# Optimization experiments

Hardware: AMD Instinct MI355X
Metric: run time of the kernel (lower is better)

## Reference

```python
import jax, jax.numpy as jnp
import numpy as np

N_NODES = 100000
N_EDGES = 1600000
D = 128
N_GRAPHS = 8


def setup_inputs() -> dict:
    key = jax.random.key(0)
    ks = jax.random.split(key, 10)
    x = jax.random.normal(ks[0], (N_NODES, D), dtype=jnp.float32)
    src = jax.random.randint(ks[1], (N_EDGES,), 0, N_NODES)
    dst = jax.random.randint(ks[2], (N_EDGES,), 0, N_NODES)
    graph_ids = jnp.sort(jax.random.randint(ks[3], (N_NODES,), 0, N_GRAPHS))
    s = 1.0 / np.sqrt(D)
    W1 = jax.random.normal(ks[4], (D, D), dtype=jnp.float32) * s
    b1 = jnp.zeros((D,), dtype=jnp.float32)
    W2 = jax.random.normal(ks[5], (D, D), dtype=jnp.float32) * s
    b2 = jnp.zeros((D,), dtype=jnp.float32)
    prelu_a = jnp.full((1,), 0.25, dtype=jnp.float32)
    lin_W = jax.random.normal(ks[6], (D, 1), dtype=jnp.float32) * s
    lin_b = jnp.zeros((1,), dtype=jnp.float32)
    return {"x": x, "src": src, "dst": dst, "graph_ids": graph_ids,
            "W1": W1, "b1": b1, "W2": W2, "b2": b2,
            "prelu_a": prelu_a, "lin_W": lin_W, "lin_b": lin_b}


def _gcn_layer(h, src, dst, n_src, n_dst, W, b):
    # GraphConv with symmetric ('both') normalization: D^{-1/2} A D^{-1/2} H W + b
    h = h @ W                                      # [N, D] small GEMM
    m = h[src] * n_src[:, None]                    # [E, D] gather (irregular)
    agg = jax.ops.segment_sum(m, dst, num_segments=N_NODES)  # scatter-add
    return agg * n_dst[:, None] + b


def reference(x, src, dst, graph_ids, W1, b1, W2, b2, prelu_a, lin_W, lin_b):
    ones_e = jnp.ones((src.shape[0],), dtype=x.dtype)
    deg_out = jnp.maximum(jax.ops.segment_sum(ones_e, src, num_segments=N_NODES), 1.0)
    deg_in = jnp.maximum(jax.ops.segment_sum(ones_e, dst, num_segments=N_NODES), 1.0)
    n_src = jax.lax.rsqrt(deg_out)[src]            # per-edge source norm
    n_dst = jax.lax.rsqrt(deg_in)                  # per-node dest norm

    h = _gcn_layer(x, src, dst, n_src, n_dst, W1, b1)
    h = jax.nn.relu(h)
    h = _gcn_layer(h, src, dst, n_src, n_dst, W2, b2)
    h = jax.nn.relu(h)

    # dgl.mean_nodes: per-graph mean over nodes
    sums = jax.ops.segment_sum(h, graph_ids, num_segments=N_GRAPHS)   # [G, D]
    cnt = jax.ops.segment_sum(jnp.ones((N_NODES,), h.dtype), graph_ids,
                              num_segments=N_GRAPHS)
    pooled = sums / jnp.maximum(cnt, 1.0)[:, None]

    # PReLU (single shared slope) -> Linear -> Sigmoid
    pooled = jnp.where(pooled > 0, pooled, prelu_a[0] * pooled)
    out = jax.nn.sigmoid(pooled @ lin_W + lin_b)   # [G, 1]
    return out
```

## Files before the change

kernel.cpp:

```cpp
#include <hip/hip_runtime.h>
#include <hip/hip_bf16.h>

#define NN 100000
#define NE 1600000
#define DD 128
#define NG 8

#define BSH 8
#define KB 391
#define BMASK 255
#define PB 512
#define CHUNK 3125
#define SCAN_N (KB * PB)
#define GHB 98

typedef unsigned short u16;
typedef unsigned char u8;
typedef __attribute__((ext_vector_type(8))) short short8;
typedef __attribute__((ext_vector_type(4))) float f32x4;
typedef __attribute__((ext_vector_type(2))) float f32x2;

static __device__ __forceinline__ u16 f2bf(float f) {
  unsigned u = __float_as_uint(f);
  u += 0x7fffu + ((u >> 16) & 1);
  return (u16)(u >> 16);
}
static __device__ __forceinline__ u8 f2fp8(float f) {
  return (u8)(__builtin_amdgcn_cvt_pk_fp8_f32(f, f, 0, false) & 0xFF);
}

__global__ __launch_bounds__(256) void p1x(const int* __restrict__ src,
                                           const int* __restrict__ dst,
                                           int* __restrict__ countsS,
                                           int* __restrict__ countsD,
                                           const float* __restrict__ W1,
                                           const float* __restrict__ W2,
                                           u16* __restrict__ Wt1,
                                           u16* __restrict__ Wt2,
                                           const int* __restrict__ gid,
                                           int* __restrict__ cnt_part,
                                           float* __restrict__ pooled) {
  __shared__ int hs[KB], hd[KB];
  __shared__ int h8[NG];
  int t = threadIdx.x, b = blockIdx.x;
  if (b < PB) {
    for (int i = t; i < KB; i += 256) { hs[i] = 0; hd[i] = 0; }
    __syncthreads();
    int e0 = b * CHUNK;
    for (int i = t; i < CHUNK; i += 256) {
      atomicAdd(&hs[src[e0 + i] >> BSH], 1);
      atomicAdd(&hd[dst[e0 + i] >> BSH], 1);
    }
    __syncthreads();
    for (int i = t; i < KB; i += 256) {
      countsS[i * PB + b] = hs[i];
      countsD[i * PB + b] = hd[i];
    }
  } else if (b < PB + 128) {
    int i = (b - PB) * 256 + t;
    if (i < DD * DD) {
      int n = i >> 7, k = i & 127;
      Wt1[i] = f2bf(W1[k * DD + n]);
    } else {
      int i2 = i - DD * DD;
      int n = i2 >> 7, k = i2 & 127;
      Wt2[i2] = f2bf(W2[k * DD + n]);
    }
  } else if (b < PB + 128 + GHB) {
    int blk = b - PB - 128;
    if (t < NG) h8[t] = 0;
    __syncthreads();
    for (int i = blk * 256 + t; i < NN; i += GHB * 256)
      atomicAdd(&h8[gid[i]], 1);
    __syncthreads();
    if (t < NG) cnt_part[blk * NG + t] = h8[t];
  } else {
    for (int i = t; i < NG * DD; i += 256) pooled[i] = 0.f;
  }
}

__global__ __launch_bounds__(256) void scanA(int* __restrict__ countsS,
                                             int* __restrict__ countsD,
                                             int* __restrict__ totS,
                                             int* __restrict__ totD) {
  __shared__ int data[PB];
  __shared__ int part[256];
  int b = blockIdx.x;
  int isS = (b < KB);
  int k = isS ? b : b - KB;
  int* counts = isS ? countsS : countsD;
  int* tot = isS ? totS : totD;
  int t = threadIdx.x;
  int* c = counts + (size_t)k * PB;
  data[t] = c[t];
  data[t + 256] = c[t + 256];
  __syncthreads();
  int a0 = data[2 * t], a1 = data[2 * t + 1];
  int s = a0 + a1;
  part[t] = s;
  __syncthreads();
  for (int off = 1; off < 256; off <<= 1) {
    int v = (t >= off) ? part[t - off] : 0;
    __syncthreads();
    part[t] += v;
    __syncthreads();
  }
  int ex = part[t] - s;
  data[2 * t] = ex;
  data[2 * t + 1] = ex + a0;
  __syncthreads();
  c[t] = data[t];
  c[t + 256] = data[t + 256];
  if (t == 255) tot[k] = part[255];
}

__global__ __launch_bounds__(256) void p2x(const int* __restrict__ src,
                                           const int* __restrict__ dst,
                                           const int* __restrict__ countsS,
                                           const int* __restrict__ countsD,
                                           const int* __restrict__ totS,
                                           const int* __restrict__ totD,
                                           int* __restrict__ baseS,
                                           int* __restrict__ baseD,
                                           u8* __restrict__ recsS,
                                           unsigned* __restrict__ recsD) {
  __shared__ int data[512];
  __shared__ int part[256];
  __shared__ int bS[KB + 1], bD[KB + 1];
  __shared__ int curS[KB], curD[KB];
  int t = threadIdx.x, blk = blockIdx.x;
#pragma unroll
  for (int pass = 0; pass < 2; ++pass) {
    const int* tot = pass ? totD : totS;
    int* bb = pass ? bD : bS;
    data[t] = (t < KB) ? tot[t] : 0;
    data[t + 256] = (t + 256 < KB) ? tot[t + 256] : 0;
    __syncthreads();
    int a0 = data[2 * t], a1 = data[2 * t + 1];
    int s = a0 + a1;
    part[t] = s;
    __syncthreads();
    for (int off = 1; off < 256; off <<= 1) {
      int v = (t >= off) ? part[t - off] : 0;
      __syncthreads();
      part[t] += v;
      __syncthreads();
    }
    int ex = part[t] - s;
    int i0 = 2 * t, i1 = 2 * t + 1;
    if (i0 <= KB) bb[i0] = ex;
    if (i1 <= KB) bb[i1] = ex + a0;
    __syncthreads();
  }
  for (int i = t; i < KB; i += 256) {
    curS[i] = countsS[i * PB + blk] + bS[i];
    curD[i] = countsD[i * PB + blk] + bD[i];
  }
  if (blk == 0) {
    for (int i = t; i <= KB; i += 256) {
      baseS[i] = bS[i];
      baseD[i] = bD[i];
    }
  }
  __syncthreads();
  int e0 = blk * CHUNK;
  for (int i = t; i < CHUNK; i += 256) {
    int s = src[e0 + i];
    int d = dst[e0 + i];
    int ps = atomicAdd(&curS[s >> BSH], 1);
    recsS[ps] = (u8)(s & BMASK);
    int pd = atomicAdd(&curD[d >> BSH], 1);
    recsD[pd] = (unsigned)s | ((unsigned)(d & BMASK) << 17);
  }
}

__global__ __launch_bounds__(256) void sd_p3x(const u8* __restrict__ recsS,
                                              const int* __restrict__ baseS,
                                              float* __restrict__ rs_out,
                                              const float* __restrict__ x,
                                              u8* __restrict__ bufA,
                                              const unsigned* __restrict__ recsD,
                                              const int* __restrict__ baseD,
                                              int* __restrict__ csr_src,
                                              int* __restrict__ cursor_end,
                                              int* __restrict__ deg_in,
                                              float* __restrict__ rs_in) {
  __shared__ int hist[256];
  __shared__ int part[256];
  __shared__ float rsl[256];
  int t = threadIdx.x;
  if (blockIdx.x < KB) {
    int k = blockIdx.x;
    int rbeg = baseS[k];
    int rend = baseS[k + 1];
    hist[t] = 0;
    __syncthreads();
    for (int i = rbeg + t; i < rend; i += 256) atomicAdd(&hist[recsS[i]], 1);
    __syncthreads();
    int nbase = k << BSH;
    int n = nbase + t;
    float rv = rsqrtf(fmaxf((float)hist[t], 1.f));
    rsl[t] = rv;
    if (n < NN) rs_out[n] = rv;
    __syncthreads();
    for (int i = t; i < 256 * 16; i += 256) {
      int row = i >> 4, c = i & 15;
      int node = nbase + row;
      if (node >= NN) break;
      float w = rsl[row];
      const float4* p = (const float4*)(x + (size_t)node * DD + c * 8);
      float4 a = p[0], b = p[1];
      int lo = 0, hi = 0;
      lo = __builtin_amdgcn_cvt_pk_fp8_f32(a.x * w, a.y * w, lo, false);
      lo = __builtin_amdgcn_cvt_pk_fp8_f32(a.z * w, a.w * w, lo, true);
      hi = __builtin_amdgcn_cvt_pk_fp8_f32(b.x * w, b.y * w, hi, false);
      hi = __builtin_amdgcn_cvt_pk_fp8_f32(b.z * w, b.w * w, hi, true);
      *(uint2*)(bufA + (size_t)node * DD + c * 8) = make_uint2((unsigned)lo, (unsigned)hi);
    }
  } else {
    int k = blockIdx.x - KB;
    int rbeg = baseD[k];
    int rend = baseD[k + 1];
    hist[t] = 0;
    __syncthreads();
    for (int i = rbeg + t; i < rend; i += 256) atomicAdd(&hist[recsD[i] >> 17], 1);
    __syncthreads();
    int h = hist[t];
    part[t] = h;
    __syncthreads();
    for (int off = 1; off < 256; off <<= 1) {
      int v = (t >= off) ? part[t - off] : 0;
      __syncthreads();
      part[t] += v;
      __syncthreads();
    }
    int run = rbeg + part[t] - h;
    int n = (k << BSH) + t;
    if (n < NN) {
      cursor_end[n] = run + h;
      deg_in[n] = h;
      rs_in[n] = rsqrtf(fmaxf((float)h, 1.f));
    }
    hist[t] = run;
    __syncthreads();
    for (int i = rbeg + t; i < rend; i += 256) {
      unsigned r = recsD[i];
      int pos = atomicAdd(&hist[r >> 17], 1);
      csr_src[pos] = (int)(r & 0x1FFFF);
    }
  }
}

__global__ __launch_bounds__(256) void gather_agg_fp8(
    const uint4* __restrict__ Hv, const int* __restrict__ csr_src,
    const int* __restrict__ cursor_end, const int* __restrict__ deg_in,
    u16* __restrict__ agg) {
  int node = blockIdx.x * 32 + (threadIdx.x >> 3);
  if (node >= NN) return;
  int q = threadIdx.x & 7;
  int end = cursor_end[node];
  int j = end - deg_in[node];
  float acc[16];
#pragma unroll
  for (int i = 0; i < 16; ++i) acc[i] = 0.f;
#define ACCV(v) { f32x2 t_;                                                        \
  t_ = __builtin_amdgcn_cvt_pk_f32_fp8((int)(v).x, false); acc[0] += t_.x;  acc[1] += t_.y;  \
  t_ = __builtin_amdgcn_cvt_pk_f32_fp8((int)(v).x, true);  acc[2] += t_.x;  acc[3] += t_.y;  \
  t_ = __builtin_amdgcn_cvt_pk_f32_fp8((int)(v).y, false); acc[4] += t_.x;  acc[5] += t_.y;  \
  t_ = __builtin_amdgcn_cvt_pk_f32_fp8((int)(v).y, true);  acc[6] += t_.x;  acc[7] += t_.y;  \
  t_ = __builtin_amdgcn_cvt_pk_f32_fp8((int)(v).z, false); acc[8] += t_.x;  acc[9] += t_.y;  \
  t_ = __builtin_amdgcn_cvt_pk_f32_fp8((int)(v).z, true);  acc[10] += t_.x; acc[11] += t_.y; \
  t_ = __builtin_amdgcn_cvt_pk_f32_fp8((int)(v).w, false); acc[12] += t_.x; acc[13] += t_.y; \
  t_ = __builtin_amdgcn_cvt_pk_f32_fp8((int)(v).w, true);  acc[14] += t_.x; acc[15] += t_.y; }
  for (; j + 4 <= end; j += 4) {
    int s0 = csr_src[j + 0];
    int s1 = csr_src[j + 1];
    int s2 = csr_src[j + 2];
    int s3 = csr_src[j + 3];
    uint4 v0 = Hv[(size_t)s0 * 8 + q];
    uint4 v1 = Hv[(size_t)s1 * 8 + q];
    uint4 v2 = Hv[(size_t)s2 * 8 + q];
    uint4 v3 = Hv[(size_t)s3 * 8 + q];
    ACCV(v0) ACCV(v1) ACCV(v2) ACCV(v3)
  }
  for (; j < end; ++j) {
    uint4 v = Hv[(size_t)csr_src[j] * 8 + q];
    ACCV(v)
  }
#undef ACCV
  uint4 o0, o1;
  o0.x = (unsigned)f2bf(acc[0])  | ((unsigned)f2bf(acc[1])  << 16);
  o0.y = (unsigned)f2bf(acc[2])  | ((unsigned)f2bf(acc[3])  << 16);
  o0.z = (unsigned)f2bf(acc[4])  | ((unsigned)f2bf(acc[5])  << 16);
  o0.w = (unsigned)f2bf(acc[6])  | ((unsigned)f2bf(acc[7])  << 16);
  o1.x = (unsigned)f2bf(acc[8])  | ((unsigned)f2bf(acc[9])  << 16);
  o1.y = (unsigned)f2bf(acc[10]) | ((unsigned)f2bf(acc[11]) << 16);
  o1.z = (unsigned)f2bf(acc[12]) | ((unsigned)f2bf(acc[13]) << 16);
  o1.w = (unsigned)f2bf(acc[14]) | ((unsigned)f2bf(acc[15]) << 16);
  u16* op = agg + (size_t)node * DD + q * 16;
  *(uint4*)op = o0;
  *(uint4*)(op + 8) = o1;
}

#define GEMM_PRE                                                              \
  __shared__ uint4 Wl4[2048];                                      \
  int tid = threadIdx.x;                                                      \
  {                                                                           \
    const uint4* Wg4 = (const uint4*)Wt;                                      \
    for (int i = tid; i < 2048; i += 256) {                                   \
      int row = i >> 4, c = i & 15;                                           \
      Wl4[(row << 4) | (c ^ (row & 15))] = Wg4[i];                            \
    }                                                                         \
  }                                                                           \
  int wid = tid >> 6;                                                         \
  int lane = tid & 63;                                                        \
  int l15 = lane & 15;                                                        \
  int kg = lane >> 4;                                                         \
  int rowbase = blockIdx.x * 128 + wid * 32;                                  \
  f32x4 acc[2][8];                                                            \
  short8 a[2][4];                                                             \
  _Pragma("unroll")                                                           \
  for (int t = 0; t < 2; ++t) {                                               \
    int arow = rowbase + t * 16 + l15;                                        \
    bool ok = arow < NN;                                                      \
    const u16* aptr = Ab + (size_t)arow * DD + kg * 8;                        \
    _Pragma("unroll")                                                         \
    for (int kt = 0; kt < 4; ++kt) {                                          \
      a[t][kt] = ok ? *(const short8*)(aptr + kt * 32)                        \
                    : (short8){0, 0, 0, 0, 0, 0, 0, 0};                       \
      acc[0][kt] = (f32x4){0.f, 0.f, 0.f, 0.f};                               \
      acc[0][kt + 4] = (f32x4){0.f, 0.f, 0.f, 0.f};                           \
      acc[1][kt] = (f32x4){0.f, 0.f, 0.f, 0.f};                               \
      acc[1][kt + 4] = (f32x4){0.f, 0.f, 0.f, 0.f};                           \
    }                                                                         \
  }                                                                           \
  __syncthreads();                                                            \
  _Pragma("unroll")                                                           \
  for (int n = 0; n < 8; ++n) {                                               \
    _Pragma("unroll")                                                         \
    for (int kt = 0; kt < 4; ++kt) {                                          \
      short8 b = *(const short8*)(Wl4 + (((n * 16 + l15) << 4) |              \
                                         ((kg + kt * 4) ^ l15)));             \
      acc[0][n] = __builtin_amdgcn_mfma_f32_16x16x32_bf16(a[0][kt], b, acc[0][n], 0, 0, 0); \
      acc[1][n] = __builtin_amdgcn_mfma_f32_16x16x32_bf16(a[1][kt], b, acc[1][n], 0, 0, 0); \
    }                                                                         \
  }

__global__ __launch_bounds__(256) void gemm_mfma_fp8out(
    const u16* __restrict__ Ab, const u16* __restrict__ Wt,
    const float* __restrict__ bias, const float* __restrict__ rs,
    const float* __restrict__ post, u8* __restrict__ Cb) {
  GEMM_PRE
#pragma unroll
  for (int t = 0; t < 2; ++t) {
    int crow0 = rowbase + t * 16 + kg * 4;
#pragma unroll
    for (int j = 0; j < 4; ++j) {
      int r = crow0 + j;
      if (r < NN) {
        float s = rs[r];
        float ps = post[r];
#pragma unroll
        for (int n = 0; n < 8; ++n) {
          float v = fmaxf(acc[t][n][j] * s + bias[n * 16 + l15], 0.f) * ps;
          Cb[(size_t)r * DD + n * 16 + l15] = f2fp8(v);
        }
      }
    }
  }
}

__global__ __launch_bounds__(256) void gemm_mfma_pool(
    const u16* __restrict__ Ab, const u16* __restrict__ Wt,
    const float* __restrict__ bias, const float* __restrict__ rs,
    const int* __restrict__ gid, float* __restrict__ pooled) {
  __shared__ float pl[NG * DD];
  for (int i = threadIdx.x; i < NG * DD; i += 256) pl[i] = 0.f;
  GEMM_PRE
  float pacc[8];
#pragma unroll
  for (int n = 0; n < 8; ++n) pacc[n] = 0.f;
  int curg = -1;
#pragma unroll
  for (int t = 0; t < 2; ++t) {
    int crow0 = rowbase + t * 16 + kg * 4;
#pragma unroll
    for (int j = 0; j < 4; ++j) {
      int r = crow0 + j;
      if (r < NN) {
        int g = gid[r];
        if (g != curg) {
          if (curg >= 0) {
#pragma unroll
            for (int n = 0; n < 8; ++n) {
              atomicAdd(&pl[curg * DD + n * 16 + l15], pacc[n]);
              pacc[n] = 0.f;
            }
          }
          curg = g;
        }
        float s = rs[r];
#pragma unroll
        for (int n = 0; n < 8; ++n)
          pacc[n] += fmaxf(acc[t][n][j] * s + bias[n * 16 + l15], 0.f);
      }
    }
  }
  if (curg >= 0) {
#pragma unroll
    for (int n = 0; n < 8; ++n)
      atomicAdd(&pl[curg * DD + n * 16 + l15], pacc[n]);
  }
  __syncthreads();
  int rlo = blockIdx.x * 128;
  int rhi = rlo + 127;
  if (rhi >= NN) rhi = NN - 1;
  int gmin = gid[rlo];
  int gmax = gid[rhi];
  int span = (gmax - gmin + 1) * DD;
  for (int i = tid; i < span; i += 256) {
    float v = pl[gmin * DD + i];
    if (v != 0.f) atomicAdd(&pooled[gmin * DD + i], v);
  }
}

__global__ __launch_bounds__(128) void final_kernel(const float* __restrict__ pooled,
                                                    const int* __restrict__ cnt_part,
                                                    const float* __restrict__ prelu_a,
                                                    const float* __restrict__ linW,
                                                    const float* __restrict__ linb,
                                                    float* __restrict__ out) {
  int t = threadIdx.x;
  __shared__ float red[2];
  __shared__ int cntl[NG];
  if (t < NG) {
    int s = 0;
    for (int b = 0; b < GHB; ++b) s += cnt_part[b * NG + t];
    cntl[t] = s;
  }
  __syncthreads();
  float w = linW[t];
  float alpha = prelu_a[0];
  float lb = linb[0];
  for (int g = 0; g < NG; ++g) {
    float v = pooled[g * DD + t] / fmaxf((float)cntl[g], 1.f);
    v = v > 0.f ? v : alpha * v;
    float p = v * w;
#pragma unroll
    for (int off = 32; off >= 1; off >>= 1) p += __shfl_down(p, off, 64);
    if ((t & 63) == 0) red[t >> 6] = p;
    __syncthreads();
    if (t == 0) {
      float s = red[0] + red[1] + lb;
      out[g] = 1.f / (1.f + expf(-s));
    }
    __syncthreads();
  }
}

extern "C" void kernel_launch(void* const* d_in, const int* in_sizes, int n_in,
                              void* d_out, int out_size, void* d_ws, size_t ws_size,
                              hipStream_t stream) {
  const float* x   = (const float*)d_in[0];
  const int*   src = (const int*)d_in[1];
  const int*   dst = (const int*)d_in[2];
  const int*   gid = (const int*)d_in[3];
  const float* W1  = (const float*)d_in[4];
  const float* b1  = (const float*)d_in[5];
  const float* W2  = (const float*)d_in[6];
  const float* b2  = (const float*)d_in[7];
  const float* pa  = (const float*)d_in[8];
  const float* lW  = (const float*)d_in[9];
  const float* lb  = (const float*)d_in[10];
  float* out = (float*)d_out;

  char* ws = (char*)d_ws;
  size_t o = 0;
  auto alloc = [&](size_t bytes) {
    size_t r = o;
    o += (bytes + 255) & ~(size_t)255;
    return r;
  };
  int*   deg_in  = (int*)(ws + alloc((size_t)NN * 4));
  float* rs_out  = (float*)(ws + alloc((size_t)NN * 4));
  float* rs_in   = (float*)(ws + alloc((size_t)NN * 4));
  int*   countsS = (int*)(ws + alloc((size_t)SCAN_N * 4));
  int*   countsD = (int*)(ws + alloc((size_t)SCAN_N * 4));
  int*   totS    = (int*)(ws + alloc((size_t)KB * 4));
  int*   totD    = (int*)(ws + alloc((size_t)KB * 4));
  int*   baseS   = (int*)(ws + alloc((size_t)(KB + 1) * 4));
  int*   baseD   = (int*)(ws + alloc((size_t)(KB + 1) * 4));
  int*   cursor_end = (int*)(ws + alloc((size_t)NN * 4));
  u8*    recsS   = (u8*)(ws + alloc((size_t)NE));
  unsigned* recsD = (unsigned*)(ws + alloc((size_t)NE * 4));
  int*   csr_src = (int*)(ws + alloc((size_t)NE * 4));
  u16*   Wt1     = (u16*)(ws + alloc((size_t)DD * DD * 2));
  u16*   Wt2     = (u16*)(ws + alloc((size_t)DD * DD * 2));
  u8*    bufA    = (u8*)(ws + alloc((size_t)NN * DD));
  u8*    bufB    = (u8*)(ws + alloc((size_t)NN * DD));
  u16*   aggbuf  = (u16*)(ws + alloc((size_t)NN * DD * 2));
  float* pooled  = (float*)(ws + alloc((size_t)NG * DD * 4));
  int*   cnt_part = (int*)(ws + alloc((size_t)GHB * NG * 4));

  p1x<<<PB + 128 + GHB + 1, 256, 0, stream>>>(src, dst, countsS, countsD,
                                              W1, W2, Wt1, Wt2, gid, cnt_part, pooled);
  scanA<<<2 * KB, 256, 0, stream>>>(countsS, countsD, totS, totD);
  p2x<<<PB, 256, 0, stream>>>(src, dst, countsS, countsD, totS, totD,
                              baseS, baseD, recsS, recsD);
  sd_p3x<<<2 * KB, 256, 0, stream>>>(recsS, baseS, rs_out, x, bufA,
                                     recsD, baseD, csr_src, cursor_end, deg_in, rs_in);

  const int gablocks = (NN + 31) / 32;
  const int gmblocks = (NN + 127) / 128;

  gather_agg_fp8<<<gablocks, 256, 0, stream>>>((const uint4*)bufA, csr_src, cursor_end, deg_in, aggbuf);
  gemm_mfma_fp8out<<<gmblocks, 256, 0, stream>>>(aggbuf, Wt1, b1, rs_in, rs_out, bufB);
  gather_agg_fp8<<<gablocks, 256, 0, stream>>>((const uint4*)bufB, csr_src, cursor_end, deg_in, aggbuf);
  gemm_mfma_pool<<<gmblocks, 256, 0, stream>>>(aggbuf, Wt2, b2, rs_in, gid, pooled);
  final_kernel<<<1, 128, 0, stream>>>(pooled, cnt_part, pa, lW, lb, out);
}
```

Baseline: 193.0 us.

## Stage bucket-scatter records in LDS before coalesced global writes

The partition kernel now first scatters each edge record into shared-memory staging arrays ordered by bucket, using a per-block local exclusive scan of the bucket counts. A second pass then copies the records to their global bucket positions, so consecutive threads write mostly contiguous addresses instead of scattered byte and word stores. This adds two more block scans, a second pass over the chunk, and a large LDS footprint, which may reduce occupancy.

```diff
diff --git a/kernel.cpp b/kernel.cpp
--- a/kernel.cpp
+++ b/kernel.cpp
@@ -114,6 +114,25 @@
   if (t == 255) tot[k] = part[255];
 }
 
+static __device__ __forceinline__ void exscan512(int t, int* data, int* part,
+                                                 int* out, int nmax) {
+  __syncthreads();
+  int a0 = data[2 * t], a1 = data[2 * t + 1];
+  int s = a0 + a1;
+  part[t] = s;
+  __syncthreads();
+  for (int off = 1; off < 256; off <<= 1) {
+    int v = (t >= off) ? part[t - off] : 0;
+    __syncthreads();
+    part[t] += v;
+    __syncthreads();
+  }
+  int ex = part[t] - s;
+  if (2 * t <= nmax) out[2 * t] = ex;
+  if (2 * t + 1 <= nmax) out[2 * t + 1] = ex + a0;
+  __syncthreads();
+}
+
 __global__ __launch_bounds__(256) void p2x(const int* __restrict__ src,
                                            const int* __restrict__ dst,
                                            const int* __restrict__ countsS,
@@ -127,50 +146,78 @@
   __shared__ int data[512];
   __shared__ int part[256];
   __shared__ int bS[KB + 1], bD[KB + 1];
-  __shared__ int curS[KB], curD[KB];
+  __shared__ int gS[KB], gD[KB];
+  __shared__ int lsS[KB + 1], lsD[KB + 1];
+  __shared__ int lcS[KB], lcD[KB];
+  __shared__ unsigned stD[CHUNK];
+  __shared__ u16 bkD[CHUNK];
+  __shared__ u8 stS[CHUNK];
+  __shared__ u16 bkS[CHUNK];
   int t = threadIdx.x, blk = blockIdx.x;
-#pragma unroll
-  for (int pass = 0; pass < 2; ++pass) {
-    const int* tot = pass ? totD : totS;
-    int* bb = pass ? bD : bS;
-    data[t] = (t < KB) ? tot[t] : 0;
-    data[t + 256] = (t + 256 < KB) ? tot[t + 256] : 0;
-    __syncthreads();
-    int a0 = data[2 * t], a1 = data[2 * t + 1];
-    int s = a0 + a1;
-    part[t] = s;
-    __syncthreads();
-    for (int off = 1; off < 256; off <<= 1) {
-      int v = (t >= off) ? part[t - off] : 0;
-      __syncthreads();
-      part[t] += v;
-      __syncthreads();
-    }
-    int ex = part[t] - s;
-    int i0 = 2 * t, i1 = 2 * t + 1;
-    if (i0 <= KB) bb[i0] = ex;
-    if (i1 <= KB) bb[i1] = ex + a0;
-    __syncthreads();
-  }
-  for (int i = t; i < KB; i += 256) {
-    curS[i] = countsS[i * PB + blk] + bS[i];
-    curD[i] = countsD[i * PB + blk] + bD[i];
-  }
+
+  data[t] = (t < KB) ? totS[t] : 0;
+  data[t + 256] = (t + 256 < KB) ? totS[t + 256] : 0;
+  exscan512(t, data, part, bS, KB);
+  data[t] = (t < KB) ? totD[t] : 0;
+  data[t + 256] = (t + 256 < KB) ? totD[t + 256] : 0;
+  exscan512(t, data, part, bD, KB);
+
   if (blk == 0) {
     for (int i = t; i <= KB; i += 256) {
       baseS[i] = bS[i];
       baseD[i] = bD[i];
     }
   }
-  __syncthreads();
+
+  for (int k = t; k < 512; k += 256) {
+    int cnt = 0;
+    if (k < KB) {
+      int pref = countsS[k * PB + blk];
+      int nxt = (blk < PB - 1) ? countsS[k * PB + blk + 1] : totS[k];
+      cnt = nxt - pref;
+      gS[k] = bS[k] + pref;
+    }
+    data[k] = cnt;
+  }
+  exscan512(t, data, part, lsS, KB);
+  for (int k = t; k < 512; k += 256) {
+    int cnt = 0;
+    if (k < KB) {
+      int pref = countsD[k * PB + blk];
+      int nxt = (blk < PB - 1) ? countsD[k * PB + blk + 1] : totD[k];
+      cnt = nxt - pref;
+      gD[k] = bD[k] + pref;
+    }
+    data[k] = cnt;
+  }
+  exscan512(t, data, part, lsD, KB);
+
+  for (int k = t; k < KB; k += 256) {
+    lcS[k] = lsS[k];
+    lcD[k] = lsD[k];
+  }
+  __syncthreads();
+
   int e0 = blk * CHUNK;
   for (int i = t; i < CHUNK; i += 256) {
     int s = src[e0 + i];
     int d = dst[e0 + i];
-    int ps = atomicAdd(&curS[s >> BSH], 1);
-    recsS[ps] = (u8)(s & BMASK);
-    int pd = atomicAdd(&curD[d >> BSH], 1);
-    recsD[pd] = (unsigned)s | ((unsigned)(d & BMASK) << 17);
+    int ks = s >> BSH;
+    int kd = d >> BSH;
+    int ps = atomicAdd(&lcS[ks], 1);
+    stS[ps] = (u8)(s & BMASK);
+    bkS[ps] = (u16)ks;
+    int pd = atomicAdd(&lcD[kd], 1);
+    stD[pd] = (unsigned)s | ((unsigned)(d & BMASK) << 17);
+    bkD[pd] = (u16)kd;
+  }
+  __syncthreads();
+
+  for (int i = t; i < CHUNK; i += 256) {
+    int kd = bkD[i];
+    recsD[gD[kd] + (i - lsD[kd])] = stD[i];
+    int ks = bkS[i];
+    recsS[gS[ks] + (i - lsS[ks])] = stS[i];
   }
 }
 
```

Measured after the change: 174.2 us, median of 2. -9.8%, faster.
